# Optimization experiments

Measured on AMD Instinct MI355X. Metric: run time of the kernel, lower is better.

The kernel has to match this reference:

```python
import jax, jax.numpy as jnp
import numpy as np
from jax import lax

H = 2048          # hidden_size
I = 1408          # moe_intermediate_size
E = 16            # n_routed_experts
K = 4             # num_experts_per_tok
N_SHARED = 2      # n_shared_experts
IS = I * N_SHARED # shared expert intermediate
B, S = 1, 1024


def setup_inputs() -> dict:
    key = jax.random.key(0)
    ks = jax.random.split(key, 8)
    scale = 0.02
    return {
        "hidden_states": jax.random.normal(ks[0], (B, S, H), dtype=jnp.float32),
        "gate_w": jax.random.normal(ks[1], (E, H), dtype=jnp.float32) * scale,  # MoEGate.weight
        "w_gate": jax.random.normal(ks[2], (E, H, I), dtype=jnp.float32) * scale,
        "w_up": jax.random.normal(ks[3], (E, H, I), dtype=jnp.float32) * scale,
        "w_down": jax.random.normal(ks[4], (E, I, H), dtype=jnp.float32) * scale,
        "sw_gate": jax.random.normal(ks[5], (H, IS), dtype=jnp.float32) * scale,
        "sw_up": jax.random.normal(ks[6], (H, IS), dtype=jnp.float32) * scale,
        "sw_down": jax.random.normal(ks[7], (IS, H), dtype=jnp.float32) * scale,
    }


def _moe_forward(hidden_states, gate_w, w_gate, w_up, w_down, sw_gate, sw_up, sw_down):
    bsz, seq_len, h = hidden_states.shape
    flat = hidden_states.reshape(-1, h)                # [T, H]
    T = flat.shape[0]

    # --- MoEGate: softmax scoring + top-k (norm_topk_prob=False) ---
    logits = flat @ gate_w.T                           # [T, E]
    scores = jax.nn.softmax(logits, axis=-1)
    topk_w, topk_idx = lax.top_k(scores, K)            # [T, K]

    # combine[t, e] = sum of top-k weights assigned to expert e (scatter of dispatch)
    combine = jnp.zeros((T, E), dtype=flat.dtype).at[
        jnp.arange(T)[:, None], topk_idx
    ].add(topk_w)                                      # [T, E]

    # --- routed experts: scan over experts, accumulate weighted SwiGLU MLP outputs ---
    def step(y, xs):
        wg, wu, wd, c = xs                             # [H,I], [H,I], [I,H], [T]
        out = (jax.nn.silu(flat @ wg) * (flat @ wu)) @ wd   # [T, H]
        return y + c[:, None] * out, None

    y, _ = lax.scan(step, jnp.zeros_like(flat), (w_gate, w_up, w_down, combine.T))

    # --- shared experts (always-on SwiGLU MLP with larger intermediate) ---
    shared = (jax.nn.silu(flat @ sw_gate) * (flat @ sw_up)) @ sw_down  # [T, H]

    return (y + shared).reshape(bsz, seq_len, h)


def reference(hidden_states, gate_w, w_gate, w_up, w_down, sw_gate, sw_up, sw_down):
    return _moe_forward(hidden_states, gate_w, w_gate, w_up, w_down,
                        sw_gate, sw_up, sw_down)
```

## Files before the change

kernel.cpp:

```cpp
#include <hip/hip_runtime.h>
#include <hip/hip_bf16.h>
#include <stdint.h>

#define T_TOK 1024
#define H_DIM 2048
#define I_DIM 1408
#define E_NUM 16
#define K_TOP 4
#define IS_DIM 2816
#define BK 64
#define BKP 72
#define BM 128
#define NT_MAX 64

typedef __hip_bfloat16 bf;
typedef __attribute__((ext_vector_type(8))) __bf16 bf16x8;
typedef __attribute__((ext_vector_type(4))) float f32x4;

__device__ __forceinline__ void gload16(const void* g, void* l) {
  __builtin_amdgcn_global_load_lds((const __attribute__((address_space(1))) void*)g,
                                   (__attribute__((address_space(3))) void*)l, 16, 0, 0);
}

__global__ void cvt_x_kernel(const float* __restrict__ in, bf* __restrict__ out) {
  int i = blockIdx.x * blockDim.x + threadIdx.x;
  float4 v = reinterpret_cast<const float4*>(in)[i];
  int b = i * 4;
  out[b + 0] = __float2bfloat16(v.x);
  out[b + 1] = __float2bfloat16(v.y);
  out[b + 2] = __float2bfloat16(v.z);
  out[b + 3] = __float2bfloat16(v.w);
}

__global__ void gate_topk_kernel(const float* __restrict__ x, const float* __restrict__ gw,
                                 int* __restrict__ topk_idx, float* __restrict__ topk_w) {
  int t = blockIdx.x;
  int lane = threadIdx.x;
  float acc[E_NUM];
#pragma unroll
  for (int e = 0; e < E_NUM; e++) acc[e] = 0.f;
  const float* xt = x + (long)t * H_DIM;
  for (int h = lane; h < H_DIM; h += 64) {
    float xv = xt[h];
#pragma unroll
    for (int e = 0; e < E_NUM; e++) acc[e] += xv * gw[e * H_DIM + h];
  }
#pragma unroll
  for (int e = 0; e < E_NUM; e++) {
    float v = acc[e];
    for (int off = 32; off; off >>= 1) v += __shfl_xor(v, off, 64);
    acc[e] = v;
  }
  if (lane == 0) {
    float m = acc[0];
#pragma unroll
    for (int e = 1; e < E_NUM; e++) m = fmaxf(m, acc[e]);
    float sc[E_NUM];
    float s = 0.f;
#pragma unroll
    for (int e = 0; e < E_NUM; e++) { sc[e] = expf(acc[e] - m); s += sc[e]; }
    float inv = 1.f / s;
#pragma unroll
    for (int e = 0; e < E_NUM; e++) sc[e] *= inv;
    for (int k = 0; k < K_TOP; k++) {
      int bi = 0;
      float bv = sc[0];
      for (int e = 1; e < E_NUM; e++)
        if (sc[e] > bv) { bv = sc[e]; bi = e; }
      topk_idx[t * K_TOP + k] = bi;
      topk_w[t * K_TOP + k] = bv;
      sc[bi] = -1.f;
    }
  }
}

__global__ void build_lists_kernel(const int* __restrict__ topk_idx,
                                   int* __restrict__ rows, int* __restrict__ tile_expert,
                                   int* __restrict__ n_tiles) {
  __shared__ int cnt[E_NUM], cur[E_NUM], s_tb;
  int tid = threadIdx.x;
  if (tid < E_NUM) cnt[tid] = 0;
  __syncthreads();
  for (int p = tid; p < T_TOK * K_TOP; p += blockDim.x)
    atomicAdd(&cnt[topk_idx[p]], 1);
  __syncthreads();
  if (tid == 0) {
    int tb = 0;
    for (int e = 0; e < E_NUM; e++) {
      int nt = (cnt[e] + BM - 1) / BM;
      cur[e] = tb * BM;
      for (int j = 0; j < nt; j++) tile_expert[tb + j] = e;
      tb += nt;
    }
    for (int j = 0; j < 16; j++) tile_expert[tb + j] = 16 + (j >> 3);
    s_tb = tb;
    *n_tiles = tb + 16;
  }
  __syncthreads();
  int tb = s_tb;
  for (int r = tid; r < NT_MAX * BM; r += blockDim.x) rows[r] = -1;
  __syncthreads();
  for (int p = tid; p < T_TOK * K_TOP; p += blockDim.x) {
    int t = p >> 2, k = p & 3;
    int e = topk_idx[p];
    int slot = atomicAdd(&cur[e], 1);
    rows[slot] = t * 8 + k;
  }
  for (int idx = tid; idx < 16 * BM; idx += blockDim.x) {
    int j = idx >> 7, r = idx & 127;
    int t = (j & 7) * BM + r;
    rows[(tb + j) * BM + r] = t * 8 + 4 + (j >> 3);
  }
}

__launch_bounds__(256, 2)
__global__ void gemm_gateup_kernel(const bf* __restrict__ xb,
                                   const int* __restrict__ rows,
                                   const int* __restrict__ tile_expert,
                                   const int* __restrict__ n_tiles,
                                   const float* __restrict__ Wg,
                                   const float* __restrict__ Wu,
                                   const float* __restrict__ SWg,
                                   const float* __restrict__ SWu,
                                   bf* __restrict__ act) {
  int bid = blockIdx.x;
  int idx = (bid & 7) * 176 + (bid >> 3);
  int x = idx >> 6, rt = idx & 63;
  if (rt >= *n_tiles) return;
  int e = tile_expert[rt];
  bool sh = e >= 16;
  const float* gbase = sh ? (SWg + (e - 16) * I_DIM) : (Wg + (long)e * H_DIM * I_DIM);
  const float* ubase = sh ? (SWu + (e - 16) * I_DIM) : (Wu + (long)e * H_DIM * I_DIM);
  long bstride = sh ? IS_DIM : I_DIM;
  int i0 = x * 64;

  __shared__ bf lA[BM * BK];
  __shared__ bf lB2[2][64 * BKP];

  int tid = threadIdx.x, w = tid >> 6, lane = tid & 63;
  int l15 = lane & 15, lhi = lane >> 4;
  int nq = tid & 15, mt = (tid >> 4) & 1, kg = tid >> 5;
  int sswz = (((lane & 7) ^ (lane >> 3)) * 8);
  int bco = (kg ^ (nq & 7)) * 8;

  const bf* asrc[4];
#pragma unroll
  for (int i = 0; i < 4; i++) {
    int rr = rt * BM + i * 32 + w * 8 + (lane >> 3);
    int p = rows[rr];
    int tok = (p >= 0) ? (p >> 3) : 0;
    asrc[i] = xb + (long)tok * H_DIM + sswz;
  }

  const float* psrc = (mt ? ubase : gbase) + i0 + nq * 4 + (long)(kg * 8) * bstride;

  f32x4 accg[4][2], accu[4][2];
  f32x4 z4 = {0.f, 0.f, 0.f, 0.f};
#pragma unroll
  for (int m = 0; m < 4; m++)
#pragma unroll
    for (int n = 0; n < 2; n++) { accg[m][n] = z4; accu[m][n] = z4; }

  int wr = w >> 1, wc = w & 1;
  for (int kt = 0; kt < H_DIM; kt += BK) {
    float4 v[8];
    const float* p_ = psrc + (long)kt * bstride;
#pragma unroll
    for (int j = 0; j < 8; j++)
      v[j] = *reinterpret_cast<const float4*>(p_ + (long)j * bstride);
    __syncthreads();
#pragma unroll
    for (int i = 0; i < 4; i++)
      gload16(asrc[i] + kt, lA + (i * 32 + w * 8) * BK);
#pragma unroll
    for (int c = 0; c < 4; c++) {
      union { bf16x8 vv; bf s[8]; } o;
#pragma unroll
      for (int j = 0; j < 8; j++)
        o.s[j] = __float2bfloat16(((const float*)&v[j])[c]);
      *reinterpret_cast<bf16x8*>(&lB2[mt][(nq * 4 + c) * BKP + bco]) = o.vv;
    }
    __syncthreads();
#pragma unroll
    for (int kk = 0; kk < 2; kk++) {
      bf16x8 af[4];
#pragma unroll
      for (int m = 0; m < 4; m++)
        af[m] = *reinterpret_cast<const bf16x8*>(
            lA + (wr * 64 + m * 16 + l15) * BK + (((kk * 4 + lhi) ^ (l15 & 7)) * 8));
#pragma unroll
      for (int n = 0; n < 2; n++) {
        int nrow = wc * 32 + n * 16 + l15;
        int bch = ((kk * 4 + lhi) ^ ((nrow >> 2) & 7)) * 8;
        bf16x8 gf = *reinterpret_cast<const bf16x8*>(&lB2[0][nrow * BKP + bch]);
        bf16x8 uf = *reinterpret_cast<const bf16x8*>(&lB2[1][nrow * BKP + bch]);
#pragma unroll
        for (int m = 0; m < 4; m++) {
          accg[m][n] = __builtin_amdgcn_mfma_f32_16x16x32_bf16(af[m], gf, accg[m][n], 0, 0, 0);
          accu[m][n] = __builtin_amdgcn_mfma_f32_16x16x32_bf16(af[m], uf, accu[m][n], 0, 0, 0);
        }
      }
    }
  }

#pragma unroll
  for (int m = 0; m < 4; m++)
#pragma unroll
    for (int n = 0; n < 2; n++)
#pragma unroll
      for (int r2 = 0; r2 < 4; r2++) {
        float gv = accg[m][n][r2];
        float uv = accu[m][n][r2];
        float s = (gv / (1.f + __expf(-gv))) * uv;
        int row = rt * BM + wr * 64 + m * 16 + lhi * 4 + r2;
        int col = i0 + wc * 32 + n * 16 + l15;
        act[(long)row * I_DIM + col] = __float2bfloat16(s);
      }
}

__launch_bounds__(256, 2)
__global__ void gemm_down_kernel(const bf* __restrict__ A,
                                 const int* __restrict__ rows,
                                 const int* __restrict__ tile_expert,
                                 const int* __restrict__ n_tiles,
                                 const float* __restrict__ Wd,
                                 const float* __restrict__ SWd,
                                 bf* __restrict__ outp) {
  int bid = blockIdx.x;
  int idx = (bid & 7) * 128 + (bid >> 3);
  int x = idx >> 6, rt = idx & 63;
  if (rt >= *n_tiles) return;
  int e = tile_expert[rt];
  bool sh = e >= 16;
  const float* bbase = sh ? (SWd + (long)(e - 16) * I_DIM * H_DIM)
                          : (Wd + (long)e * I_DIM * H_DIM);
  int h0 = x * 128;

  __shared__ bf lA[BM * BK];
  __shared__ bf lB[128 * BKP];
  __shared__ int rowsl[BM];

  int tid = threadIdx.x, w = tid >> 6, lane = tid & 63;
  int l15 = lane & 15, lhi = lane >> 4;
  int kg = tid >> 5, ng = tid & 31;
  int sswz = (((lane & 7) ^ (lane >> 3)) * 8);
  int bco = (kg ^ (ng & 7)) * 8;
  if (tid < BM) rowsl[tid] = rows[rt * BM + tid];

  const bf* asrc[4];
#pragma unroll
  for (int i = 0; i < 4; i++)
    asrc[i] = A + (long)(rt * BM + i * 32 + w * 8 + (lane >> 3)) * I_DIM + sswz;

  const float* psrc = bbase + h0 + ng * 4 + (long)(kg * 8) * H_DIM;

  f32x4 acc[4][4];
  f32x4 z4 = {0.f, 0.f, 0.f, 0.f};
#pragma unroll
  for (int m = 0; m < 4; m++)
#pragma unroll
    for (int n = 0; n < 4; n++) acc[m][n] = z4;

  int wr = w >> 1, wc = w & 1;
  for (int kt = 0; kt < I_DIM; kt += BK) {
    float4 v[8];
    const float* p_ = psrc + (long)kt * H_DIM;
#pragma unroll
    for (int j = 0; j < 8; j++)
      v[j] = *reinterpret_cast<const float4*>(p_ + (long)j * H_DIM);
    __syncthreads();
#pragma unroll
    for (int i = 0; i < 4; i++)
      gload16(asrc[i] + kt, lA + (i * 32 + w * 8) * BK);
#pragma unroll
    for (int c = 0; c < 4; c++) {
      union { bf16x8 vv; bf s[8]; } o;
#pragma unroll
      for (int j = 0; j < 8; j++)
        o.s[j] = __float2bfloat16(((const float*)&v[j])[c]);
      *reinterpret_cast<bf16x8*>(&lB[(ng * 4 + c) * BKP + bco]) = o.vv;
    }
    __syncthreads();
#pragma unroll
    for (int kk = 0; kk < 2; kk++) {
      bf16x8 af[4];
#pragma unroll
      for (int m = 0; m < 4; m++)
        af[m] = *reinterpret_cast<const bf16x8*>(
            lA + (wr * 64 + m * 16 + l15) * BK + (((kk * 4 + lhi) ^ (l15 & 7)) * 8));
#pragma unroll
      for (int n = 0; n < 4; n++) {
        int nrow = wc * 64 + n * 16 + l15;
        int bch = ((kk * 4 + lhi) ^ ((nrow >> 2) & 7)) * 8;
        bf16x8 bfr = *reinterpret_cast<const bf16x8*>(&lB[nrow * BKP + bch]);
#pragma unroll
        for (int m = 0; m < 4; m++)
          acc[m][n] = __builtin_amdgcn_mfma_f32_16x16x32_bf16(af[m], bfr, acc[m][n], 0, 0, 0);
      }
    }
  }

#pragma unroll
  for (int m = 0; m < 4; m++)
#pragma unroll
    for (int n = 0; n < 4; n++)
#pragma unroll
      for (int r2 = 0; r2 < 4; r2++) {
        int lrow = wr * 64 + m * 16 + lhi * 4 + r2;
        int col = h0 + wc * 64 + n * 16 + l15;
        int p = rowsl[lrow];
        if (p >= 0) outp[(long)p * H_DIM + col] = __float2bfloat16(acc[m][n][r2]);
      }
}

__global__ void combine_kernel(const bf* __restrict__ outp,
                               const float* __restrict__ topk_w,
                               float* __restrict__ out) {
  int g = blockIdx.x * blockDim.x + threadIdx.x;
  int t = g >> 8;
  int h = (g & 255) * 8;
  const bf* base = outp + (long)t * 8 * H_DIM + h;
  float w0 = topk_w[t * 4 + 0], w1 = topk_w[t * 4 + 1];
  float w2 = topk_w[t * 4 + 2], w3 = topk_w[t * 4 + 3];
  bf16x8 s4 = *reinterpret_cast<const bf16x8*>(base + 4 * H_DIM);
  bf16x8 s5 = *reinterpret_cast<const bf16x8*>(base + 5 * H_DIM);
  bf16x8 r0 = *reinterpret_cast<const bf16x8*>(base + 0 * H_DIM);
  bf16x8 r1 = *reinterpret_cast<const bf16x8*>(base + 1 * H_DIM);
  bf16x8 r2 = *reinterpret_cast<const bf16x8*>(base + 2 * H_DIM);
  bf16x8 r3 = *reinterpret_cast<const bf16x8*>(base + 3 * H_DIM);
  float acc[8];
#pragma unroll
  for (int j = 0; j < 8; j++) {
    acc[j] = (float)s4[j] + (float)s5[j]
           + w0 * (float)r0[j] + w1 * (float)r1[j]
           + w2 * (float)r2[j] + w3 * (float)r3[j];
  }
  float4* o = reinterpret_cast<float4*>(out + (long)t * H_DIM + h);
  o[0] = make_float4(acc[0], acc[1], acc[2], acc[3]);
  o[1] = make_float4(acc[4], acc[5], acc[6], acc[7]);
}

extern "C" void kernel_launch(void* const* d_in, const int* in_sizes, int n_in,
                              void* d_out, int out_size, void* d_ws, size_t ws_size,
                              hipStream_t stream) {
  const float* x     = (const float*)d_in[0];
  const float* gw    = (const float*)d_in[1];
  const float* wgate = (const float*)d_in[2];
  const float* wup   = (const float*)d_in[3];
  const float* wdown = (const float*)d_in[4];
  const float* swg   = (const float*)d_in[5];
  const float* swu   = (const float*)d_in[6];
  const float* swd   = (const float*)d_in[7];
  float* out = (float*)d_out;

  char* ws = (char*)d_ws;
  size_t off = 0;
  auto alloc = [&](size_t bytes) {
    void* p = ws + off;
    off += (bytes + 255) & ~(size_t)255;
    return p;
  };

  bf* xb   = (bf*)alloc((size_t)T_TOK * H_DIM * 2);
  bf* act  = (bf*)alloc((size_t)NT_MAX * BM * I_DIM * 2);
  bf* outp = (bf*)alloc((size_t)T_TOK * 8 * H_DIM * 2);
  int*   topk_idx = (int*)alloc(T_TOK * K_TOP * 4);
  float* topk_w   = (float*)alloc(T_TOK * K_TOP * 4);
  int*   rowsbuf  = (int*)alloc(NT_MAX * BM * 4);
  int*   tile_exp = (int*)alloc(NT_MAX * 4);
  int*   n_tiles  = (int*)alloc(64);
  (void)ws_size; (void)in_sizes; (void)n_in; (void)out_size;

  hipLaunchKernelGGL(cvt_x_kernel, dim3(T_TOK * H_DIM / 1024), dim3(256), 0, stream, x, xb);
  hipLaunchKernelGGL(gate_topk_kernel, dim3(T_TOK), dim3(64), 0, stream, x, gw, topk_idx, topk_w);
  hipLaunchKernelGGL(build_lists_kernel, dim3(1), dim3(256), 0, stream, topk_idx, rowsbuf, tile_exp, n_tiles);

  hipLaunchKernelGGL(gemm_gateup_kernel, dim3((I_DIM / 64) * NT_MAX), dim3(256), 0, stream,
                     xb, rowsbuf, tile_exp, n_tiles, wgate, wup, swg, swu, act);
  hipLaunchKernelGGL(gemm_down_kernel, dim3((H_DIM / 128) * NT_MAX), dim3(256), 0, stream,
                     act, rowsbuf, tile_exp, n_tiles, wdown, swd, outp);

  hipLaunchKernelGGL(combine_kernel, dim3(T_TOK * H_DIM / 8 / 256), dim3(256), 0, stream,
                     outp, topk_w, out);
}
```

Measured before the change: 320.6 us.

## Double row tile to 256 with 512-thread blocks in MoE GEMMs

Raises the token-row tile from 128 to 256 and launches 512-thread blocks, so each fp32 weight tile is loaded and converted to bf16 once per 256 gathered rows instead of once per 128. The weight staging is split across two half-groups of threads, each loading four k-rows and writing 4-element bf16 chunks into LDS. Tile lists, shared-expert tiles and grid swizzles are resized to match. The cost is more padding waste per expert and a tighter per-thread register budget under the new launch bounds, which may cause spills.

Measured after the change: 321.9 us. No clear change (+0.4%).

```diff
diff --git a/kernel.cpp b/kernel.cpp
--- a/kernel.cpp
+++ b/kernel.cpp
@@ -10,8 +10,8 @@
 #define IS_DIM 2816
 #define BK 64
 #define BKP 72
-#define BM 128
-#define NT_MAX 64
+#define BM 256
+#define NT_MAX 40
 
 typedef __hip_bfloat16 bf;
 typedef __attribute__((ext_vector_type(8))) __bf16 bf16x8;
@@ -92,9 +92,9 @@
       for (int j = 0; j < nt; j++) tile_expert[tb + j] = e;
       tb += nt;
     }
-    for (int j = 0; j < 16; j++) tile_expert[tb + j] = 16 + (j >> 3);
+    for (int j = 0; j < 8; j++) tile_expert[tb + j] = 16 + (j >> 2);
     s_tb = tb;
-    *n_tiles = tb + 16;
+    *n_tiles = tb + 8;
   }
   __syncthreads();
   int tb = s_tb;
@@ -106,14 +106,14 @@
     int slot = atomicAdd(&cur[e], 1);
     rows[slot] = t * 8 + k;
   }
-  for (int idx = tid; idx < 16 * BM; idx += blockDim.x) {
-    int j = idx >> 7, r = idx & 127;
-    int t = (j & 7) * BM + r;
-    rows[(tb + j) * BM + r] = t * 8 + 4 + (j >> 3);
-  }
-}
-
-__launch_bounds__(256, 2)
+  for (int idx = tid; idx < 8 * BM; idx += blockDim.x) {
+    int j = idx >> 8, r = idx & 255;
+    int t = (j & 3) * BM + r;
+    rows[(tb + j) * BM + r] = t * 8 + 4 + (j >> 2);
+  }
+}
+
+__launch_bounds__(512, 4)
 __global__ void gemm_gateup_kernel(const bf* __restrict__ xb,
                                    const int* __restrict__ rows,
                                    const int* __restrict__ tile_expert,
@@ -124,8 +124,8 @@
                                    const float* __restrict__ SWu,
                                    bf* __restrict__ act) {
   int bid = blockIdx.x;
-  int idx = (bid & 7) * 176 + (bid >> 3);
-  int x = idx >> 6, rt = idx & 63;
+  int idx = (bid & 7) * 110 + (bid >> 3);
+  int x = idx / NT_MAX, rt = idx % NT_MAX;
   if (rt >= *n_tiles) return;
   int e = tile_expert[rt];
   bool sh = e >= 16;
@@ -139,20 +139,20 @@
 
   int tid = threadIdx.x, w = tid >> 6, lane = tid & 63;
   int l15 = lane & 15, lhi = lane >> 4;
-  int nq = tid & 15, mt = (tid >> 4) & 1, kg = tid >> 5;
+  int nq = tid & 15, mt = (tid >> 4) & 1, kq = (tid >> 5) & 7, jh = tid >> 8;
   int sswz = (((lane & 7) ^ (lane >> 3)) * 8);
-  int bco = (kg ^ (nq & 7)) * 8;
+  int bco = (kq ^ (nq & 7)) * 8 + jh * 4;
 
   const bf* asrc[4];
 #pragma unroll
   for (int i = 0; i < 4; i++) {
-    int rr = rt * BM + i * 32 + w * 8 + (lane >> 3);
+    int rr = rt * BM + i * 64 + w * 8 + (lane >> 3);
     int p = rows[rr];
     int tok = (p >= 0) ? (p >> 3) : 0;
     asrc[i] = xb + (long)tok * H_DIM + sswz;
   }
 
-  const float* psrc = (mt ? ubase : gbase) + i0 + nq * 4 + (long)(kg * 8) * bstride;
+  const float* psrc = (mt ? ubase : gbase) + i0 + nq * 4 + (long)(kq * 8 + jh * 4) * bstride;
 
   f32x4 accg[4][2], accu[4][2];
   f32x4 z4 = {0.f, 0.f, 0.f, 0.f};
@@ -163,22 +163,22 @@
 
   int wr = w >> 1, wc = w & 1;
   for (int kt = 0; kt < H_DIM; kt += BK) {
-    float4 v[8];
+    float4 v[4];
     const float* p_ = psrc + (long)kt * bstride;
 #pragma unroll
-    for (int j = 0; j < 8; j++)
+    for (int j = 0; j < 4; j++)
       v[j] = *reinterpret_cast<const float4*>(p_ + (long)j * bstride);
     __syncthreads();
 #pragma unroll
     for (int i = 0; i < 4; i++)
-      gload16(asrc[i] + kt, lA + (i * 32 + w * 8) * BK);
+      gload16(asrc[i] + kt, lA + (i * 64 + w * 8) * BK);
 #pragma unroll
     for (int c = 0; c < 4; c++) {
-      union { bf16x8 vv; bf s[8]; } o;
-#pragma unroll
-      for (int j = 0; j < 8; j++)
-        o.s[j] = __float2bfloat16(((const float*)&v[j])[c]);
-      *reinterpret_cast<bf16x8*>(&lB2[mt][(nq * 4 + c) * BKP + bco]) = o.vv;
+      union { short4 s4; bf b[4]; } o;
+#pragma unroll
+      for (int j = 0; j < 4; j++)
+        o.b[j] = __float2bfloat16(((const float*)&v[j])[c]);
+      *reinterpret_cast<short4*>(&lB2[mt][(nq * 4 + c) * BKP + bco]) = o.s4;
     }
     __syncthreads();
 #pragma unroll
@@ -218,7 +218,7 @@
       }
 }
 
-__launch_bounds__(256, 2)
+__launch_bounds__(512, 4)
 __global__ void gemm_down_kernel(const bf* __restrict__ A,
                                  const int* __restrict__ rows,
                                  const int* __restrict__ tile_expert,
@@ -227,8 +227,8 @@
                                  const float* __restrict__ SWd,
                                  bf* __restrict__ outp) {
   int bid = blockIdx.x;
-  int idx = (bid & 7) * 128 + (bid >> 3);
-  int x = idx >> 6, rt = idx & 63;
+  int idx = (bid & 7) * 80 + (bid >> 3);
+  int x = idx / NT_MAX, rt = idx % NT_MAX;
   if (rt >= *n_tiles) return;
   int e = tile_expert[rt];
   bool sh = e >= 16;
@@ -242,17 +242,17 @@
 
   int tid = threadIdx.x, w = tid >> 6, lane = tid & 63;
   int l15 = lane & 15, lhi = lane >> 4;
-  int kg = tid >> 5, ng = tid & 31;
+  int ng = tid & 31, kq = (tid >> 5) & 7, jh = tid >> 8;
   int sswz = (((lane & 7) ^ (lane >> 3)) * 8);
-  int bco = (kg ^ (ng & 7)) * 8;
+  int bco = (kq ^ (ng & 7)) * 8 + jh * 4;
   if (tid < BM) rowsl[tid] = rows[rt * BM + tid];
 
   const bf* asrc[4];
 #pragma unroll
   for (int i = 0; i < 4; i++)
-    asrc[i] = A + (long)(rt * BM + i * 32 + w * 8 + (lane >> 3)) * I_DIM + sswz;
-
-  const float* psrc = bbase + h0 + ng * 4 + (long)(kg * 8) * H_DIM;
+    asrc[i] = A + (long)(rt * BM + i * 64 + w * 8 + (lane >> 3)) * I_DIM + sswz;
+
+  const float* psrc = bbase + h0 + ng * 4 + (long)(kq * 8 + jh * 4) * H_DIM;
 
   f32x4 acc[4][4];
   f32x4 z4 = {0.f, 0.f, 0.f, 0.f};
@@ -263,22 +263,22 @@
 
   int wr = w >> 1, wc = w & 1;
   for (int kt = 0; kt < I_DIM; kt += BK) {
-    float4 v[8];
+    float4 v[4];
     const float* p_ = psrc + (long)kt * H_DIM;
 #pragma unroll
-    for (int j = 0; j < 8; j++)
+    for (int j = 0; j < 4; j++)
       v[j] = *reinterpret_cast<const float4*>(p_ + (long)j * H_DIM);
     __syncthreads();
 #pragma unroll
     for (int i = 0; i < 4; i++)
-      gload16(asrc[i] + kt, lA + (i * 32 + w * 8) * BK);
+      gload16(asrc[i] + kt, lA + (i * 64 + w * 8) * BK);
 #pragma unroll
     for (int c = 0; c < 4; c++) {
-      union { bf16x8 vv; bf s[8]; } o;
-#pragma unroll
-      for (int j = 0; j < 8; j++)
-        o.s[j] = __float2bfloat16(((const float*)&v[j])[c]);
-      *reinterpret_cast<bf16x8*>(&lB[(ng * 4 + c) * BKP + bco]) = o.vv;
+      union { short4 s4; bf b[4]; } o;
+#pragma unroll
+      for (int j = 0; j < 4; j++)
+        o.b[j] = __float2bfloat16(((const float*)&v[j])[c]);
+      *reinterpret_cast<short4*>(&lB[(ng * 4 + c) * BKP + bco]) = o.s4;
     }
     __syncthreads();
 #pragma unroll
@@ -375,9 +375,9 @@
   hipLaunchKernelGGL(gate_topk_kernel, dim3(T_TOK), dim3(64), 0, stream, x, gw, topk_idx, topk_w);
   hipLaunchKernelGGL(build_lists_kernel, dim3(1), dim3(256), 0, stream, topk_idx, rowsbuf, tile_exp, n_tiles);
 
-  hipLaunchKernelGGL(gemm_gateup_kernel, dim3((I_DIM / 64) * NT_MAX), dim3(256), 0, stream,
+  hipLaunchKernelGGL(gemm_gateup_kernel, dim3(22 * NT_MAX), dim3(512), 0, stream,
                      xb, rowsbuf, tile_exp, n_tiles, wgate, wup, swg, swu, act);
-  hipLaunchKernelGGL(gemm_down_kernel, dim3((H_DIM / 128) * NT_MAX), dim3(256), 0, stream,
+  hipLaunchKernelGGL(gemm_down_kernel, dim3(16 * NT_MAX), dim3(512), 0, stream,
                      act, rowsbuf, tile_exp, n_tiles, wdown, swd, outp);
 
   hipLaunchKernelGGL(combine_kernel, dim3(T_TOK * H_DIM / 8 / 256), dim3(256), 0, stream,
```
